# Kernel tuning notes

Measured on AMD Instinct MI355X. Metric: run time of the kernel, lower is better.

## Reference

```python
import jax, jax.numpy as jnp
import numpy as np

N_SYM, N_DIS, F_IN, HID, OUT, E = 50000, 10000, 128, 128, 64, 640000
NEG_SLOPE = 0.2


def _gat(x_src, x_dst, src, dst, Ws, Wd, a_s, a_d, b, n_dst):
    # PyG GATConv (bipartite, heads=1, add_self_loops=False)
    h_src = x_src @ Ws                      # [Ns, H]
    h_dst = x_dst @ Wd                      # [Nd, H]
    al = h_src @ a_s                        # [Ns]
    ar = h_dst @ a_d                        # [Nd]
    e = jax.nn.leaky_relu(al[src] + ar[dst], NEG_SLOPE)   # [E]
    m = jax.ops.segment_max(e, dst, num_segments=n_dst)   # per-dst max
    ex = jnp.exp(e - m[dst])
    den = jax.ops.segment_sum(ex, dst, num_segments=n_dst)
    alpha = ex / den[dst]                   # segment softmax over in-edges
    out = jax.ops.segment_sum(alpha[:, None] * h_src[src], dst, num_segments=n_dst)
    return out + b


def setup_inputs() -> dict:
    key = jax.random.key(0)
    ks = jax.random.split(key, 16)
    s = 0.05
    return {
        'x_sym': jax.random.normal(ks[0], (N_SYM, F_IN), jnp.float32),
        'x_dis': jax.random.normal(ks[1], (N_DIS, F_IN), jnp.float32),
        'edge_src': jax.random.randint(ks[2], (E,), 0, N_SYM, jnp.int32),
        'edge_dst': jax.random.randint(ks[3], (E,), 0, N_DIS, jnp.int32),
        'Wsrc_sd': jax.random.normal(ks[4], (F_IN, HID), jnp.float32) * s,
        'Wdst_sd': jax.random.normal(ks[5], (F_IN, HID), jnp.float32) * s,
        'asrc_sd': jax.random.normal(ks[6], (HID,), jnp.float32) * s,
        'adst_sd': jax.random.normal(ks[7], (HID,), jnp.float32) * s,
        'b_sd': jax.random.normal(ks[8], (HID,), jnp.float32) * s,
        'Wsrc_ds': jax.random.normal(ks[9], (F_IN, HID), jnp.float32) * s,
        'Wdst_ds': jax.random.normal(ks[10], (F_IN, HID), jnp.float32) * s,
        'asrc_ds': jax.random.normal(ks[11], (HID,), jnp.float32) * s,
        'adst_ds': jax.random.normal(ks[12], (HID,), jnp.float32) * s,
        'b_ds': jax.random.normal(ks[13], (HID,), jnp.float32) * s,
        'lin_W': jax.random.normal(ks[14], (HID, OUT), jnp.float32) * s,
        'lin_b': jax.random.normal(ks[15], (OUT,), jnp.float32) * s,
    }


def reference(x_sym, x_dis, edge_src, edge_dst,
              Wsrc_sd, Wdst_sd, asrc_sd, adst_sd, b_sd,
              Wsrc_ds, Wdst_ds, asrc_ds, adst_ds, b_ds,
              lin_W, lin_b):
    # symptom -> disease edge type
    h_dis = _gat(x_sym, x_dis, edge_src, edge_dst,
                 Wsrc_sd, Wdst_sd, asrc_sd, adst_sd, b_sd, N_DIS)
    # disease -> symptom (reverse edges)
    h_sym = _gat(x_dis, x_sym, edge_dst, edge_src,
                 Wsrc_ds, Wdst_ds, asrc_ds, adst_ds, b_ds, N_SYM)
    h_sym = jax.nn.relu(h_sym)  # only symptom branch feeds lin
    return h_sym @ lin_W + lin_b
```

## Files before the change

### kernel.cpp

```cpp
#include <hip/hip_runtime.h>
#include <hip/hip_fp16.h>

#define N_SYM 50000
#define N_DIS 10000
#define F_IN 128
#define HID 128
#define OUTF 64
#define NE 640000
#define NEG_SLOPE 0.2f

#define SPAN 128
#define NB 391
#define SUBS 16
#define SCAP 192
#define CURSTRIDE 16
#define NREG (NB * SUBS)
#define LCAP 48
#define HSTR 144

#define AR_BLOCKS 6250
#define PROJ_BLOCKS 625

typedef _Float16 f16x8 __attribute__((ext_vector_type(8)));
typedef float f32x4 __attribute__((ext_vector_type(4)));

__global__ __launch_bounds__(256) void k_pre(const float* __restrict__ Wd,
                                             const float* __restrict__ ad,
                                             float* __restrict__ v_dst,
                                             int* __restrict__ bcur) {
    int tid = threadIdx.x;
    for (int i = blockIdx.x * 256 + tid; i < NREG * CURSTRIDE; i += 64 * 256)
        bcur[i] = 0;
    if (blockIdx.x == 0) {
        int k = tid >> 1;
        int hh = tid & 1;
        const float4* Wr = (const float4*)(Wd + k * HID + hh * 64);
        const float4* av = (const float4*)(ad + hh * 64);
        float s = 0.f;
#pragma unroll
        for (int j = 0; j < 16; ++j) {
            float4 w = Wr[j], xx = av[j];
            s += w.x * xx.x + w.y * xx.y + w.z * xx.z + w.w * xx.w;
        }
        s += __shfl_xor(s, 1);
        if (!hh) v_dst[k] = s;
    }
}

#define R1 16
__global__ __launch_bounds__(256) void k_main(const float* __restrict__ x_sym,
                                              const float* __restrict__ x_dis,
                                              const int* __restrict__ esrc,
                                              const int* __restrict__ edst,
                                              const float* __restrict__ Wsrc,
                                              const float* __restrict__ asrc,
                                              const float* __restrict__ v_dst,
                                              __half* __restrict__ h16,
                                              float* __restrict__ al2,
                                              float* __restrict__ ar2,
                                              int* __restrict__ bcur,
                                              unsigned int* __restrict__ bins) {
    int tid = threadIdx.x;
    if (blockIdx.x < AR_BLOCKS) {
        int gid = blockIdx.x * 256 + tid;
        if (gid < NE) {
            int s = esrc[gid];
            int d = edst[gid];
            int region = (s >> 7) * SUBS + (blockIdx.x & (SUBS - 1));
            unsigned int v = ((unsigned int)(s & 127) << 14) | (unsigned int)d;
            int pos = atomicAdd(&bcur[region * CURSTRIDE], 1);
            if (pos < SCAP) bins[region * SCAP + pos] = v;
        }
        int r = gid >> 5;
        int l = tid & 31;
        if (r >= N_SYM) return;
        float4 hv = *(const float4*)(x_sym + r * F_IN + l * 4);
        float4 av = *(const float4*)(v_dst + l * 4);
        float s = hv.x * av.x + hv.y * av.y + hv.z * av.z + hv.w * av.w;
#pragma unroll
        for (int m = 16; m; m >>= 1) s += __shfl_xor(s, m);
        if (!l) ar2[r] = s;
        return;
    }
    int pblk = blockIdx.x - AR_BLOCKS;
    __shared__ float xl[R1 * F_IN];
    int rowbase = pblk * R1;
    const float4* src = (const float4*)(x_dis + rowbase * F_IN);
    float4* dl = (float4*)xl;
    for (int i = tid; i < R1 * F_IN / 4; i += 256) dl[i] = src[i];
    __syncthreads();
    int c2 = tid & 63;
    int rg = tid >> 6;
    float acc[4][2] = {};
    for (int k = 0; k < F_IN; ++k) {
        float2 w = *(const float2*)(Wsrc + k * HID + c2 * 2);
#pragma unroll
        for (int i = 0; i < 4; ++i) {
            float xv = xl[(rg + 4 * i) * F_IN + k];
            acc[i][0] += xv * w.x;
            acc[i][1] += xv * w.y;
        }
    }
    __half2* h2 = (__half2*)h16;
    float2 av = *(const float2*)(asrc + 2 * c2);
#pragma unroll
    for (int i = 0; i < 4; ++i) {
        h2[(rowbase + rg + 4 * i) * 64 + c2] = __floats2half2_rn(acc[i][0], acc[i][1]);
        float p = acc[i][0] * av.x + acc[i][1] * av.y;
#pragma unroll
        for (int m = 32; m; m >>= 1) p += __shfl_xor(p, m);
        if (c2 == 0) al2[rowbase + rg + 4 * i] = p;
    }
}

__device__ __forceinline__ void acc_row(float4& acc, float2 rr, float ww) {
    __half2 a01 = *(__half2*)&rr.x;
    __half2 a23 = *(__half2*)&rr.y;
    float2 f01 = __half22float2(a01), f23 = __half22float2(a23);
    acc.x += ww * f01.x;
    acc.y += ww * f01.y;
    acc.z += ww * f23.x;
    acc.w += ww * f23.y;
}

__global__ __launch_bounds__(512) void k_fuse(const unsigned int* __restrict__ bins,
                                              const int* __restrict__ bcur,
                                              const float* __restrict__ al2,
                                              const float* __restrict__ ar2,
                                              const __half* __restrict__ h16,
                                              const float* __restrict__ b_ds,
                                              const float* __restrict__ lin_W,
                                              const float* __restrict__ lin_b,
                                              float* __restrict__ out) {
    __shared__ int lcount[SPAN];
    __shared__ unsigned short lb[SPAN * LCAP];
    __shared__ __align__(16) _Float16 htile[SPAN][HSTR];
    __shared__ __align__(16) _Float16 BT[OUTF][HSTR];
    __shared__ float bias[OUTF];
    int tid = threadIdx.x;
    int bin = blockIdx.x;
    int nodebase = bin * SPAN;
    int nnodes = min(SPAN, N_SYM - nodebase);
    for (int i = tid; i < SPAN; i += 512) lcount[i] = 0;
    for (int idx = tid; idx < HID * OUTF; idx += 512) {
        int k = idx >> 6, c = idx & 63;
        BT[c][k] = (_Float16)lin_W[idx];
    }
    if (tid < OUTF) bias[tid] = lin_b[tid];
    __syncthreads();
    {
        int hw = tid >> 5;
        int hl = tid & 31;
        int region = bin * SUBS + hw;
        int n = bcur[region * CURSTRIDE];
        if (n > SCAP) n = SCAP;
        const unsigned int* base = bins + region * SCAP;
        for (int i = hl; i < n; i += 32) {
            unsigned int v = base[i];
            int sl = v >> 14;
            int d = v & 0x3FFF;
            int rank = atomicAdd(&lcount[sl], 1);
            if (rank < LCAP) lb[sl * LCAP + rank] = (unsigned short)d;
        }
    }
    __syncthreads();
    int wave = tid >> 6, lane = tid & 63, half = lane >> 5, l = lane & 31;
    const float2* hb = (const float2*)h16;
    for (int p = 0; p < 8; ++p) {
        int nl = p * 16 + wave * 2 + half;
        if (nl >= nnodes) continue;
        int dg = min(lcount[nl], LCAP);
        int off = nl * LCAP;
        float arn = ar2[nodebase + nl];
        int di = 0;
        float lv = -1e30f;
        if (l < dg) {
            di = lb[off + l];
            float t = al2[di] + arn;
            lv = (t > 0.f) ? t : NEG_SLOPE * t;
        }
        float mm = lv;
        for (int i = 32 + l; i < dg; i += 32) {
            float t = al2[lb[off + i]] + arn;
            t = (t > 0.f) ? t : NEG_SLOPE * t;
            mm = fmaxf(mm, t);
        }
#pragma unroll
        for (int s = 16; s; s >>= 1) mm = fmaxf(mm, __shfl_xor(mm, s, 32));
        float4 acc = make_float4(0.f, 0.f, 0.f, 0.f);
        float den = 0.f;
        int dgc = dg < 32 ? dg : 32;
        int e = 0;
        for (; e + 4 <= dgc; e += 4) {
            int d0 = __shfl(di, e + 0, 32); float w0 = __expf(__shfl(lv, e + 0, 32) - mm);
            int d1 = __shfl(di, e + 1, 32); float w1 = __expf(__shfl(lv, e + 1, 32) - mm);
            int d2 = __shfl(di, e + 2, 32); float w2 = __expf(__shfl(lv, e + 2, 32) - mm);
            int d3 = __shfl(di, e + 3, 32); float w3 = __expf(__shfl(lv, e + 3, 32) - mm);
            float2 r0 = hb[d0 * 32 + l];
            float2 r1 = hb[d1 * 32 + l];
            float2 r2 = hb[d2 * 32 + l];
            float2 r3 = hb[d3 * 32 + l];
            den += w0 + w1 + w2 + w3;
            acc_row(acc, r0, w0);
            acc_row(acc, r1, w1);
            acc_row(acc, r2, w2);
            acc_row(acc, r3, w3);
        }
        for (; e < dgc; ++e) {
            int d = __shfl(di, e, 32);
            float w = __expf(__shfl(lv, e, 32) - mm);
            float2 r = hb[d * 32 + l];
            den += w;
            acc_row(acc, r, w);
        }
        for (int i = 32; i < dg; ++i) {
            int dd = lb[off + i];
            float t = al2[dd] + arn;
            t = (t > 0.f) ? t : NEG_SLOPE * t;
            float w = __expf(t - mm);
            float2 r = hb[dd * 32 + l];
            den += w;
            acc_row(acc, r, w);
        }
        float inv = (dg > 0) ? 1.f / den : 0.f;
        float4 bv = *(const float4*)(b_ds + l * 4);
        __half2 o01 = __floats2half2_rn(fmaxf(acc.x * inv + bv.x, 0.f),
                                        fmaxf(acc.y * inv + bv.y, 0.f));
        __half2 o23 = __floats2half2_rn(fmaxf(acc.z * inv + bv.z, 0.f),
                                        fmaxf(acc.w * inv + bv.w, 0.f));
        float2 pack;
        *(__half2*)&pack.x = o01;
        *(__half2*)&pack.y = o23;
        *(float2*)&htile[nl][l * 4] = pack;
    }
    __syncthreads();
    int rowloc = wave * 16 + (lane & 15);
    int kbase = (lane >> 4) * 8;
    f16x8 a[4];
#pragma unroll
    for (int kc = 0; kc < 4; ++kc)
        a[kc] = *(const f16x8*)(&htile[rowloc][kc * 32 + kbase]);
#pragma unroll
    for (int ct = 0; ct < 4; ++ct) {
        int bcol = ct * 16 + (lane & 15);
        f32x4 acc = {0.f, 0.f, 0.f, 0.f};
#pragma unroll
        for (int kc = 0; kc < 4; ++kc) {
            f16x8 bf = *(const f16x8*)(&BT[bcol][kc * 32 + kbase]);
            acc = __builtin_amdgcn_mfma_f32_16x16x32_f16(a[kc], bf, acc, 0, 0, 0);
        }
        int r0 = wave * 16 + (lane >> 4) * 4;
        float bc = bias[bcol];
#pragma unroll
        for (int r = 0; r < 4; ++r) {
            int rl = r0 + r;
            if (rl < nnodes) out[(nodebase + rl) * OUTF + bcol] = acc[r] + bc;
        }
    }
}

extern "C" void kernel_launch(void* const* d_in, const int* in_sizes, int n_in,
                              void* d_out, int out_size, void* d_ws, size_t ws_size,
                              hipStream_t stream) {
    const float* x_sym   = (const float*)d_in[0];
    const float* x_dis   = (const float*)d_in[1];
    const int*   esrc    = (const int*)d_in[2];
    const int*   edst    = (const int*)d_in[3];
    const float* Wsrc_ds = (const float*)d_in[9];
    const float* Wdst_ds = (const float*)d_in[10];
    const float* asrc_ds = (const float*)d_in[11];
    const float* adst_ds = (const float*)d_in[12];
    const float* b_ds    = (const float*)d_in[13];
    const float* lin_W   = (const float*)d_in[14];
    const float* lin_b   = (const float*)d_in[15];
    float* out = (float*)d_out;

    float*  ws     = (float*)d_ws;
    float*  v_dst  = ws;
    float*  al2    = v_dst + 128;
    float*  ar2    = al2 + N_DIS;
    int*    bcur   = (int*)(ar2 + N_SYM);
    unsigned int* bins = (unsigned int*)(bcur + NREG * CURSTRIDE);
    __half* h16    = (__half*)(bins + NREG * SCAP);

    k_pre<<<64, 256, 0, stream>>>(Wdst_ds, adst_ds, v_dst, bcur);
    k_main<<<AR_BLOCKS + PROJ_BLOCKS, 256, 0, stream>>>(x_sym, x_dis, esrc, edst,
                                                        Wsrc_ds, asrc_ds, v_dst,
                                                        h16, al2, ar2, bcur, bins);
    k_fuse<<<NB, 512, 0, stream>>>(bins, bcur, al2, ar2, h16, b_ds,
                                   lin_W, lin_b, out);
}
```

Baseline: 95.63 us.

## Replace global atomic edge binning with block-local counting sort kernel

Edge binning moves out of the projection kernel into a dedicated sort kernel. Each block counts its 4000-edge chunk per 128-node bin in shared memory, scans the counts, scatters locally, then reserves space with one global atomic per bin and writes contiguous runs. This removes the per-edge global atomics and the 16-way sub-region split, and the fuse kernel now reads one bin per block. The gather loop is also restructured to batch 8 shuffles and loads per round, but it adds a kernel launch and a serial dependency before the main kernel.

```diff
diff --git a/kernel.cpp b/kernel.cpp
--- a/kernel.cpp
+++ b/kernel.cpp
@@ -10,13 +10,13 @@
 #define NEG_SLOPE 0.2f
 
 #define SPAN 128
-#define NB 391
-#define SUBS 16
-#define SCAP 192
-#define CURSTRIDE 16
-#define NREG (NB * SUBS)
+#define NBIN 391
+#define BCAP 2048
+#define CSTRIDE 16
 #define LCAP 48
 #define HSTR 144
+#define CHUNK 4000
+#define NSORT 160
 
 #define AR_BLOCKS 6250
 #define PROJ_BLOCKS 625
@@ -27,10 +27,10 @@
 __global__ __launch_bounds__(256) void k_pre(const float* __restrict__ Wd,
                                              const float* __restrict__ ad,
                                              float* __restrict__ v_dst,
-                                             int* __restrict__ bcur) {
+                                             int* __restrict__ bincnt) {
     int tid = threadIdx.x;
-    for (int i = blockIdx.x * 256 + tid; i < NREG * CURSTRIDE; i += 64 * 256)
-        bcur[i] = 0;
+    for (int i = blockIdx.x * 256 + tid; i < NBIN * CSTRIDE; i += 32 * 256)
+        bincnt[i] = 0;
     if (blockIdx.x == 0) {
         int k = tid >> 1;
         int hh = tid & 1;
@@ -47,30 +47,77 @@
     }
 }
 
+__global__ __launch_bounds__(256) void k_sort(const int* __restrict__ esrc,
+                                              const int* __restrict__ edst,
+                                              int* __restrict__ bincnt,
+                                              unsigned int* __restrict__ bins) {
+    __shared__ int lcnt[NBIN];
+    __shared__ int lexcl[NBIN + 1];
+    __shared__ int lcur[NBIN];
+    __shared__ int lgbase[NBIN];
+    __shared__ unsigned int sorted[CHUNK];
+    int tid = threadIdx.x;
+    int base = blockIdx.x * CHUNK;
+    for (int i = tid; i < NBIN; i += 256) lcnt[i] = 0;
+    __syncthreads();
+    for (int i = tid; i < CHUNK; i += 256)
+        atomicAdd(&lcnt[esrc[base + i] >> 7], 1);
+    __syncthreads();
+    if (tid < 64) {
+        int run = 0;
+#pragma unroll
+        for (int c = 0; c < 7; ++c) {
+            int idx = c * 64 + tid;
+            int v = (idx < NBIN) ? lcnt[idx] : 0;
+            int x = v;
+#pragma unroll
+            for (int d = 1; d < 64; d <<= 1) {
+                int y = __shfl_up(x, d);
+                if (tid >= d) x += y;
+            }
+            if (idx < NBIN) lexcl[idx] = run + x - v;
+            run += __shfl(x, 63);
+        }
+        if (tid == 0) lexcl[NBIN] = run;
+    }
+    __syncthreads();
+    for (int i = tid; i < NBIN; i += 256) lcur[i] = lexcl[i];
+    __syncthreads();
+    for (int i = tid; i < CHUNK; i += 256) {
+        int s = esrc[base + i];
+        int d = edst[base + i];
+        int b = s >> 7;
+        int pos = atomicAdd(&lcur[b], 1);
+        sorted[pos] = ((unsigned int)(s & 127) << 14) | (unsigned int)d;
+    }
+    for (int b = tid; b < NBIN; b += 256) {
+        int c = lcnt[b];
+        lgbase[b] = c ? atomicAdd(&bincnt[b * CSTRIDE], c) : 0;
+    }
+    __syncthreads();
+    for (int i = tid; i < CHUNK; i += 256) {
+        int lo = 0, hi = NBIN;
+        while (hi - lo > 1) {
+            int mid = (lo + hi) >> 1;
+            if (lexcl[mid] <= i) lo = mid; else hi = mid;
+        }
+        int off = lgbase[lo] + (i - lexcl[lo]);
+        if (off < BCAP) bins[lo * BCAP + off] = sorted[i];
+    }
+}
+
 #define R1 16
-__global__ __launch_bounds__(256) void k_main(const float* __restrict__ x_sym,
-                                              const float* __restrict__ x_dis,
-                                              const int* __restrict__ esrc,
-                                              const int* __restrict__ edst,
-                                              const float* __restrict__ Wsrc,
-                                              const float* __restrict__ asrc,
-                                              const float* __restrict__ v_dst,
-                                              __half* __restrict__ h16,
-                                              float* __restrict__ al2,
-                                              float* __restrict__ ar2,
-                                              int* __restrict__ bcur,
-                                              unsigned int* __restrict__ bins) {
+__global__ __launch_bounds__(256) void k_main2(const float* __restrict__ x_sym,
+                                               const float* __restrict__ x_dis,
+                                               const float* __restrict__ Wsrc,
+                                               const float* __restrict__ asrc,
+                                               const float* __restrict__ v_dst,
+                                               __half* __restrict__ h16,
+                                               float* __restrict__ al2,
+                                               float* __restrict__ ar2) {
     int tid = threadIdx.x;
     if (blockIdx.x < AR_BLOCKS) {
         int gid = blockIdx.x * 256 + tid;
-        if (gid < NE) {
-            int s = esrc[gid];
-            int d = edst[gid];
-            int region = (s >> 7) * SUBS + (blockIdx.x & (SUBS - 1));
-            unsigned int v = ((unsigned int)(s & 127) << 14) | (unsigned int)d;
-            int pos = atomicAdd(&bcur[region * CURSTRIDE], 1);
-            if (pos < SCAP) bins[region * SCAP + pos] = v;
-        }
         int r = gid >> 5;
         int l = tid & 31;
         if (r >= N_SYM) return;
@@ -124,7 +171,7 @@
 }
 
 __global__ __launch_bounds__(512) void k_fuse(const unsigned int* __restrict__ bins,
-                                              const int* __restrict__ bcur,
+                                              const int* __restrict__ bincnt,
                                               const float* __restrict__ al2,
                                               const float* __restrict__ ar2,
                                               const __half* __restrict__ h16,
@@ -149,13 +196,9 @@
     if (tid < OUTF) bias[tid] = lin_b[tid];
     __syncthreads();
     {
-        int hw = tid >> 5;
-        int hl = tid & 31;
-        int region = bin * SUBS + hw;
-        int n = bcur[region * CURSTRIDE];
-        if (n > SCAP) n = SCAP;
-        const unsigned int* base = bins + region * SCAP;
-        for (int i = hl; i < n; i += 32) {
+        int n = min(bincnt[bin * CSTRIDE], BCAP);
+        const unsigned int* base = bins + bin * BCAP;
+        for (int i = tid; i < n; i += 512) {
             unsigned int v = base[i];
             int sl = v >> 14;
             int d = v & 0x3FFF;
@@ -190,28 +233,24 @@
         float4 acc = make_float4(0.f, 0.f, 0.f, 0.f);
         float den = 0.f;
         int dgc = dg < 32 ? dg : 32;
-        int e = 0;
-        for (; e + 4 <= dgc; e += 4) {
-            int d0 = __shfl(di, e + 0, 32); float w0 = __expf(__shfl(lv, e + 0, 32) - mm);
-            int d1 = __shfl(di, e + 1, 32); float w1 = __expf(__shfl(lv, e + 1, 32) - mm);
-            int d2 = __shfl(di, e + 2, 32); float w2 = __expf(__shfl(lv, e + 2, 32) - mm);
-            int d3 = __shfl(di, e + 3, 32); float w3 = __expf(__shfl(lv, e + 3, 32) - mm);
-            float2 r0 = hb[d0 * 32 + l];
-            float2 r1 = hb[d1 * 32 + l];
-            float2 r2 = hb[d2 * 32 + l];
-            float2 r3 = hb[d3 * 32 + l];
-            den += w0 + w1 + w2 + w3;
-            acc_row(acc, r0, w0);
-            acc_row(acc, r1, w1);
-            acc_row(acc, r2, w2);
-            acc_row(acc, r3, w3);
-        }
-        for (; e < dgc; ++e) {
-            int d = __shfl(di, e, 32);
-            float w = __expf(__shfl(lv, e, 32) - mm);
-            float2 r = hb[d * 32 + l];
-            den += w;
-            acc_row(acc, r, w);
+        int rounds = (dgc + 7) >> 3;
+        for (int rd = 0; rd < rounds; ++rd) {
+            int e0 = rd * 8;
+            int dA[8];
+            float wA[8];
+            float2 rA[8];
+#pragma unroll
+            for (int j = 0; j < 8; ++j) {
+                dA[j] = __shfl(di, e0 + j, 32);
+                wA[j] = __expf(__shfl(lv, e0 + j, 32) - mm);
+            }
+#pragma unroll
+            for (int j = 0; j < 8; ++j) rA[j] = hb[dA[j] * 32 + l];
+#pragma unroll
+            for (int j = 0; j < 8; ++j) {
+                den += wA[j];
+                acc_row(acc, rA[j], wA[j]);
+            }
         }
         for (int i = 32; i < dg; ++i) {
             int dd = lb[off + i];
@@ -279,14 +318,15 @@
     float*  v_dst  = ws;
     float*  al2    = v_dst + 128;
     float*  ar2    = al2 + N_DIS;
-    int*    bcur   = (int*)(ar2 + N_SYM);
-    unsigned int* bins = (unsigned int*)(bcur + NREG * CURSTRIDE);
-    __half* h16    = (__half*)(bins + NREG * SCAP);
-
-    k_pre<<<64, 256, 0, stream>>>(Wdst_ds, adst_ds, v_dst, bcur);
-    k_main<<<AR_BLOCKS + PROJ_BLOCKS, 256, 0, stream>>>(x_sym, x_dis, esrc, edst,
-                                                        Wsrc_ds, asrc_ds, v_dst,
-                                                        h16, al2, ar2, bcur, bins);
-    k_fuse<<<NB, 512, 0, stream>>>(bins, bcur, al2, ar2, h16, b_ds,
-                                   lin_W, lin_b, out);
-}
+    int*    bincnt = (int*)(ar2 + N_SYM);
+    unsigned int* bins = (unsigned int*)(bincnt + NBIN * CSTRIDE);
+    __half* h16    = (__half*)(bins + NBIN * BCAP);
+
+    k_pre<<<32, 256, 0, stream>>>(Wdst_ds, adst_ds, v_dst, bincnt);
+    k_sort<<<NSORT, 256, 0, stream>>>(esrc, edst, bincnt, bins);
+    k_main2<<<AR_BLOCKS + PROJ_BLOCKS, 256, 0, stream>>>(x_sym, x_dis, Wsrc_ds,
+                                                         asrc_ds, v_dst, h16,
+                                                         al2, ar2);
+    k_fuse<<<NBIN, 512, 0, stream>>>(bins, bincnt, al2, ar2, h16, b_ds,
+                                     lin_W, lin_b, out);
+}
```

New measurement: 101.5 us. +6.1%, slower.

## Bucket edges per source node with striped counters instead of per-region bins

Applied to the files above, without the earlier changes.

Edge binning now keys on the exact source node, using 8 striped counters per node with 16 slots each. This replaces the old per-region 32-bit bins and the shared-memory re-scatter in the fused kernel, which now copies small per-node buckets straight into LDS. The projection and the v_dst computation move into one kernel. The ar/binning pass is now a separate launch that depends on v_dst, instead of running concurrently with the projection. The gather loop is restructured to issue eight row loads before accumulating, to raise memory-level parallelism. The cost is more atomics on scattered counters, a larger counter array to zero, and capacity truncation if a stripe gets more than 16 edges for one node.

```diff
diff --git a/kernel.cpp b/kernel.cpp
--- a/kernel.cpp
+++ b/kernel.cpp
@@ -9,29 +9,29 @@
 #define NE 640000
 #define NEG_SLOPE 0.2f
 
+#define NX 8
+#define SCAPX 16
+#define LCAP 48
 #define SPAN 128
-#define NB 391
-#define SUBS 16
-#define SCAP 192
-#define CURSTRIDE 16
-#define NREG (NB * SUBS)
-#define LCAP 48
+#define NBIN 391
 #define HSTR 144
-
-#define AR_BLOCKS 6250
-#define PROJ_BLOCKS 625
 
 typedef _Float16 f16x8 __attribute__((ext_vector_type(8)));
 typedef float f32x4 __attribute__((ext_vector_type(4)));
 
-__global__ __launch_bounds__(256) void k_pre(const float* __restrict__ Wd,
-                                             const float* __restrict__ ad,
-                                             float* __restrict__ v_dst,
-                                             int* __restrict__ bcur) {
+#define R1 16
+__global__ __launch_bounds__(256) void k_proj(const float* __restrict__ x,
+                                              const float* __restrict__ W,
+                                              const float* __restrict__ asrc,
+                                              const float* __restrict__ Wd,
+                                              const float* __restrict__ ad,
+                                              __half* __restrict__ h,
+                                              float* __restrict__ al2,
+                                              float* __restrict__ v_dst,
+                                              int* __restrict__ cnt) {
     int tid = threadIdx.x;
-    for (int i = blockIdx.x * 256 + tid; i < NREG * CURSTRIDE; i += 64 * 256)
-        bcur[i] = 0;
-    if (blockIdx.x == 0) {
+    for (int i = blockIdx.x * 256 + tid; i < NX * N_SYM; i += 626 * 256) cnt[i] = 0;
+    if (blockIdx.x == 625) {
         int k = tid >> 1;
         int hh = tid & 1;
         const float4* Wr = (const float4*)(Wd + k * HID + hh * 64);
@@ -44,48 +44,11 @@
         }
         s += __shfl_xor(s, 1);
         if (!hh) v_dst[k] = s;
-    }
-}
-
-#define R1 16
-__global__ __launch_bounds__(256) void k_main(const float* __restrict__ x_sym,
-                                              const float* __restrict__ x_dis,
-                                              const int* __restrict__ esrc,
-                                              const int* __restrict__ edst,
-                                              const float* __restrict__ Wsrc,
-                                              const float* __restrict__ asrc,
-                                              const float* __restrict__ v_dst,
-                                              __half* __restrict__ h16,
-                                              float* __restrict__ al2,
-                                              float* __restrict__ ar2,
-                                              int* __restrict__ bcur,
-                                              unsigned int* __restrict__ bins) {
-    int tid = threadIdx.x;
-    if (blockIdx.x < AR_BLOCKS) {
-        int gid = blockIdx.x * 256 + tid;
-        if (gid < NE) {
-            int s = esrc[gid];
-            int d = edst[gid];
-            int region = (s >> 7) * SUBS + (blockIdx.x & (SUBS - 1));
-            unsigned int v = ((unsigned int)(s & 127) << 14) | (unsigned int)d;
-            int pos = atomicAdd(&bcur[region * CURSTRIDE], 1);
-            if (pos < SCAP) bins[region * SCAP + pos] = v;
-        }
-        int r = gid >> 5;
-        int l = tid & 31;
-        if (r >= N_SYM) return;
-        float4 hv = *(const float4*)(x_sym + r * F_IN + l * 4);
-        float4 av = *(const float4*)(v_dst + l * 4);
-        float s = hv.x * av.x + hv.y * av.y + hv.z * av.z + hv.w * av.w;
-#pragma unroll
-        for (int m = 16; m; m >>= 1) s += __shfl_xor(s, m);
-        if (!l) ar2[r] = s;
         return;
     }
-    int pblk = blockIdx.x - AR_BLOCKS;
     __shared__ float xl[R1 * F_IN];
-    int rowbase = pblk * R1;
-    const float4* src = (const float4*)(x_dis + rowbase * F_IN);
+    int rowbase = blockIdx.x * R1;
+    const float4* src = (const float4*)(x + rowbase * F_IN);
     float4* dl = (float4*)xl;
     for (int i = tid; i < R1 * F_IN / 4; i += 256) dl[i] = src[i];
     __syncthreads();
@@ -93,7 +56,7 @@
     int rg = tid >> 6;
     float acc[4][2] = {};
     for (int k = 0; k < F_IN; ++k) {
-        float2 w = *(const float2*)(Wsrc + k * HID + c2 * 2);
+        float2 w = *(const float2*)(W + k * HID + c2 * 2);
 #pragma unroll
         for (int i = 0; i < 4; ++i) {
             float xv = xl[(rg + 4 * i) * F_IN + k];
@@ -101,7 +64,7 @@
             acc[i][1] += xv * w.y;
         }
     }
-    __half2* h2 = (__half2*)h16;
+    __half2* h2 = (__half2*)h;
     float2 av = *(const float2*)(asrc + 2 * c2);
 #pragma unroll
     for (int i = 0; i < 4; ++i) {
@@ -111,6 +74,33 @@
         for (int m = 32; m; m >>= 1) p += __shfl_xor(p, m);
         if (c2 == 0) al2[rowbase + rg + 4 * i] = p;
     }
+}
+
+__global__ __launch_bounds__(256) void k_ar(const float* __restrict__ h,
+                                            const float* __restrict__ a,
+                                            float* __restrict__ o,
+                                            const int* __restrict__ esrc,
+                                            const int* __restrict__ edst,
+                                            int* __restrict__ cnt,
+                                            unsigned short* __restrict__ bucketx) {
+    int gid = blockIdx.x * 256 + threadIdx.x;
+    if (gid < NE) {
+        int s = esrc[gid];
+        int d = edst[gid];
+        int x = blockIdx.x & (NX - 1);
+        int cell = x * N_SYM + s;
+        int rank = atomicAdd(&cnt[cell], 1);
+        if (rank < SCAPX) bucketx[cell * SCAPX + rank] = (unsigned short)d;
+    }
+    int r = gid >> 5;
+    int l = threadIdx.x & 31;
+    if (r >= N_SYM) return;
+    float4 hv = *(const float4*)(h + r * F_IN + l * 4);
+    float4 av = *(const float4*)(a + l * 4);
+    float s = hv.x * av.x + hv.y * av.y + hv.z * av.z + hv.w * av.w;
+#pragma unroll
+    for (int m = 16; m; m >>= 1) s += __shfl_xor(s, m);
+    if (!l) o[r] = s;
 }
 
 __device__ __forceinline__ void acc_row(float4& acc, float2 rr, float ww) {
@@ -123,8 +113,8 @@
     acc.w += ww * f23.y;
 }
 
-__global__ __launch_bounds__(512) void k_fuse(const unsigned int* __restrict__ bins,
-                                              const int* __restrict__ bcur,
+__global__ __launch_bounds__(512) void k_fuse(const int* __restrict__ cnt,
+                                              const unsigned short* __restrict__ bucketx,
                                               const float* __restrict__ al2,
                                               const float* __restrict__ ar2,
                                               const __half* __restrict__ h16,
@@ -132,6 +122,7 @@
                                               const float* __restrict__ lin_W,
                                               const float* __restrict__ lin_b,
                                               float* __restrict__ out) {
+    __shared__ int cntl[SPAN][NX];
     __shared__ int lcount[SPAN];
     __shared__ unsigned short lb[SPAN * LCAP];
     __shared__ __align__(16) _Float16 htile[SPAN][HSTR];
@@ -147,20 +138,23 @@
         BT[c][k] = (_Float16)lin_W[idx];
     }
     if (tid < OUTF) bias[tid] = lin_b[tid];
-    __syncthreads();
-    {
-        int hw = tid >> 5;
-        int hl = tid & 31;
-        int region = bin * SUBS + hw;
-        int n = bcur[region * CURSTRIDE];
-        if (n > SCAP) n = SCAP;
-        const unsigned int* base = bins + region * SCAP;
-        for (int i = hl; i < n; i += 32) {
-            unsigned int v = base[i];
-            int sl = v >> 14;
-            int d = v & 0x3FFF;
-            int rank = atomicAdd(&lcount[sl], 1);
-            if (rank < LCAP) lb[sl * LCAP + rank] = (unsigned short)d;
+    for (int i = tid; i < SPAN * NX; i += 512) {
+        int node = i & (SPAN - 1);
+        int x = i >> 7;
+        int v = (node < nnodes) ? cnt[x * N_SYM + nodebase + node] : 0;
+        cntl[node][x] = (v > SCAPX) ? SCAPX : v;
+    }
+    __syncthreads();
+    for (int i = tid; i < SPAN * NX; i += 512) {
+        int node = i & (SPAN - 1);
+        int x = i >> 7;
+        int n = cntl[node][x];
+        if (n <= 0 || node >= nnodes) continue;
+        int base = atomicAdd(&lcount[node], n);
+        const unsigned short* cell = bucketx + (x * N_SYM + nodebase + node) * SCAPX;
+        for (int j = 0; j < n; ++j) {
+            int idx = base + j;
+            if (idx < LCAP) lb[node * LCAP + idx] = cell[j];
         }
     }
     __syncthreads();
@@ -190,28 +184,24 @@
         float4 acc = make_float4(0.f, 0.f, 0.f, 0.f);
         float den = 0.f;
         int dgc = dg < 32 ? dg : 32;
-        int e = 0;
-        for (; e + 4 <= dgc; e += 4) {
-            int d0 = __shfl(di, e + 0, 32); float w0 = __expf(__shfl(lv, e + 0, 32) - mm);
-            int d1 = __shfl(di, e + 1, 32); float w1 = __expf(__shfl(lv, e + 1, 32) - mm);
-            int d2 = __shfl(di, e + 2, 32); float w2 = __expf(__shfl(lv, e + 2, 32) - mm);
-            int d3 = __shfl(di, e + 3, 32); float w3 = __expf(__shfl(lv, e + 3, 32) - mm);
-            float2 r0 = hb[d0 * 32 + l];
-            float2 r1 = hb[d1 * 32 + l];
-            float2 r2 = hb[d2 * 32 + l];
-            float2 r3 = hb[d3 * 32 + l];
-            den += w0 + w1 + w2 + w3;
-            acc_row(acc, r0, w0);
-            acc_row(acc, r1, w1);
-            acc_row(acc, r2, w2);
-            acc_row(acc, r3, w3);
-        }
-        for (; e < dgc; ++e) {
-            int d = __shfl(di, e, 32);
-            float w = __expf(__shfl(lv, e, 32) - mm);
-            float2 r = hb[d * 32 + l];
-            den += w;
-            acc_row(acc, r, w);
+        int rounds = (dgc + 7) >> 3;
+        for (int rd = 0; rd < rounds; ++rd) {
+            int e0 = rd * 8;
+            int dA[8];
+            float wA[8];
+            float2 rA[8];
+#pragma unroll
+            for (int j = 0; j < 8; ++j) {
+                dA[j] = __shfl(di, e0 + j, 32);
+                wA[j] = __expf(__shfl(lv, e0 + j, 32) - mm);
+            }
+#pragma unroll
+            for (int j = 0; j < 8; ++j) rA[j] = hb[dA[j] * 32 + l];
+#pragma unroll
+            for (int j = 0; j < 8; ++j) {
+                den += wA[j];
+                acc_row(acc, rA[j], wA[j]);
+            }
         }
         for (int i = 32; i < dg; ++i) {
             int dd = lb[off + i];
@@ -279,14 +269,14 @@
     float*  v_dst  = ws;
     float*  al2    = v_dst + 128;
     float*  ar2    = al2 + N_DIS;
-    int*    bcur   = (int*)(ar2 + N_SYM);
-    unsigned int* bins = (unsigned int*)(bcur + NREG * CURSTRIDE);
-    __half* h16    = (__half*)(bins + NREG * SCAP);
-
-    k_pre<<<64, 256, 0, stream>>>(Wdst_ds, adst_ds, v_dst, bcur);
-    k_main<<<AR_BLOCKS + PROJ_BLOCKS, 256, 0, stream>>>(x_sym, x_dis, esrc, edst,
-                                                        Wsrc_ds, asrc_ds, v_dst,
-                                                        h16, al2, ar2, bcur, bins);
-    k_fuse<<<NB, 512, 0, stream>>>(bins, bcur, al2, ar2, h16, b_ds,
-                                   lin_W, lin_b, out);
-}
+    int*    cnt    = (int*)(ar2 + N_SYM);
+    unsigned short* bucketx = (unsigned short*)(cnt + NX * N_SYM);
+    __half* h16    = (__half*)(bucketx + NX * N_SYM * SCAPX);
+
+    k_proj<<<626, 256, 0, stream>>>(x_dis, Wsrc_ds, asrc_ds, Wdst_ds, adst_ds,
+                                    h16, al2, v_dst, cnt);
+    k_ar<<<N_SYM * 32 / 256, 256, 0, stream>>>(x_sym, v_dst, ar2, esrc, edst,
+                                               cnt, bucketx);
+    k_fuse<<<NBIN, 512, 0, stream>>>(cnt, bucketx, al2, ar2, h16, b_ds,
+                                     lin_W, lin_b, out);
+}
```

Measured after the change: 88.91 us. -7.0%, faster.
